# Performance work log

Hardware: AMD Instinct MI355X
Metric: run time of the kernel (lower is better)

Reference implementation:

```python
import jax, jax.numpy as jnp
import numpy as np

N_NODES = 30000
N_EDGES = 480000
T_STEPS = 8
F_IN = 8
HID = 32
K = 5
PERIODS = 8


def setup_inputs() -> dict:
    key = jax.random.key(0)
    ks = jax.random.split(key, 9)
    timesteps = jax.random.normal(ks[0], (T_STEPS, N_NODES, F_IN), jnp.float32)
    src = jax.random.randint(ks[1], (N_EDGES,), 0, N_NODES)
    dst = jax.random.randint(ks[2], (N_EDGES,), 0, N_NODES)
    edge_index = jnp.stack([src, dst])
    # ChebConv weights for gates [i, f, c, o]; glorot-ish scale
    Wx = jax.random.normal(ks[3], (4, K, F_IN, HID), jnp.float32) * (1.0 / np.sqrt(F_IN))
    Wh = jax.random.normal(ks[4], (4, K, HID, HID), jnp.float32) * (1.0 / np.sqrt(HID))
    w_c = jax.random.normal(ks[5], (3, HID), jnp.float32) * 0.1  # peepholes for i, f, o
    b_gates = jax.random.normal(ks[6], (4, HID), jnp.float32) * 0.1  # b_i, b_f, b_c, b_o
    W_lin = jax.random.normal(ks[7], (PERIODS, HID), jnp.float32) * (1.0 / np.sqrt(HID))
    b_lin = jax.random.normal(ks[8], (PERIODS,), jnp.float32) * 0.1
    return {"timesteps": timesteps, "edge_index": edge_index, "Wx": Wx, "Wh": Wh,
            "w_c": w_c, "b_gates": b_gates, "W_lin": W_lin, "b_lin": b_lin}


def reference(timesteps, edge_index, Wx, Wh, w_c, b_gates, W_lin, b_lin):
    N = timesteps.shape[1]
    src, dst = edge_index[0], edge_index[1]
    # get_laplacian('sym') removes self loops, deg over edge rows; with lambda_max=2,
    # L_hat = 2L/lmax - I = -D^{-1/2} A D^{-1/2} (diag: 1 from L plus added -1 self loop = 0)
    w = jnp.where(src != dst, 1.0, 0.0).astype(timesteps.dtype)
    deg = jax.ops.segment_sum(w, src, num_segments=N)
    dis = jnp.where(deg > 0, 1.0 / jnp.sqrt(jnp.where(deg > 0, deg, 1.0)), 0.0)
    norm = dis[src] * w * dis[dst]  # [E]

    def lap(x):  # x: [N, C] -> L_hat @ x
        return -jax.ops.segment_sum(norm[:, None] * x[src], dst, num_segments=N)

    def cheb(x, W):  # Chebyshev recurrence; W: [K, in, out]
        Tx0 = x
        out = Tx0 @ W[0]
        Tx1 = lap(Tx0)
        out = out + Tx1 @ W[1]
        for k in range(2, W.shape[0]):
            Tx2 = 2.0 * lap(Tx1) - Tx0
            out = out + Tx2 @ W[k]
            Tx0, Tx1 = Tx1, Tx2
        return out

    def step(carry, x):
        H, C = carry
        I = jax.nn.sigmoid(cheb(x, Wx[0]) + cheb(H, Wh[0]) + w_c[0] * C + b_gates[0])
        Fg = jax.nn.sigmoid(cheb(x, Wx[1]) + cheb(H, Wh[1]) + w_c[1] * C + b_gates[1])
        Tg = jnp.tanh(cheb(x, Wx[2]) + cheb(H, Wh[2]) + b_gates[2])
        Cn = Fg * C + I * Tg
        O = jax.nn.sigmoid(cheb(x, Wx[3]) + cheb(H, Wh[3]) + w_c[2] * Cn + b_gates[3])
        Hn = O * jnp.tanh(Cn)
        return (Hn, Cn), None

    hid = Wh.shape[-1]
    H0 = jnp.zeros((N, hid), timesteps.dtype)
    (H, C), _ = jax.lax.scan(step, (H0, H0), timesteps)
    return jax.nn.relu(H) @ W_lin.T + b_lin
```

## Files before the change

kernel.cpp:

```cpp
#include <hip/hip_runtime.h>
#include <hip/hip_fp16.h>
#include <math.h>

#define T_STEPS 8
#define F_IN    8
#define HID     32
#define KCH     5
#define PERIODS 8
#define NB      64

typedef __attribute__((ext_vector_type(8))) _Float16 half8_t;
typedef __attribute__((ext_vector_type(4))) float    f32x4_t;

__device__ __forceinline__ float sigmoidf_(float x) { return 1.f / (1.f + __expf(-x)); }
__device__ __forceinline__ float tanhf_(float x) {
    float e = __expf(2.f * x);
    return 1.f - 2.f / (e + 1.f);
}


__global__ void k_count(const int* __restrict__ src, const int* __restrict__ dst,
                        int* __restrict__ degi, int* __restrict__ cnt, int E) {
    int e = blockIdx.x * blockDim.x + threadIdx.x;
    if (e >= E) return;
    int s = src[e], d = dst[e];
    if (s != d) {
        atomicAdd(&degi[s], 1);
        atomicAdd(&cnt[d], 1);
    }
}

__global__ void k_hist2(const int* __restrict__ cnt, int* __restrict__ hist,
                        int N, int NT) {
    __shared__ int h[256];
    int tid = threadIdx.x, blk = blockIdx.x;
    h[tid] = 0;
    __syncthreads();
    int n = blk * 256 + tid;
    if (n < N) atomicAdd(&h[min(cnt[n], 255)], 1);
    __syncthreads();
    hist[tid * NT + blk] = h[tid];
}

__global__ void __launch_bounds__(1024) k_scan(const int* __restrict__ in,
                                               int* __restrict__ outp, int n) {
    __shared__ int wsum[16];
    int tid = threadIdx.x;
    int base = tid * 32;
    int v[32];
    int s = 0;
    #pragma unroll
    for (int i = 0; i < 32; ++i) {
        int idx = base + i;
        int t = (idx < n) ? in[idx] : 0;
        v[i] = t; s += t;
    }
    int lane = tid & 63, wave = tid >> 6;
    int incl = s;
    #pragma unroll
    for (int off = 1; off < 64; off <<= 1) {
        int t = __shfl_up(incl, off, 64);
        if (lane >= off) incl += t;
    }
    if (lane == 63) wsum[wave] = incl;
    __syncthreads();
    if (tid < 64) {
        int w = (tid < 16) ? wsum[tid] : 0;
        int iw = w;
        #pragma unroll
        for (int off = 1; off < 16; off <<= 1) {
            int t = __shfl_up(iw, off, 64);
            if (tid >= off) iw += t;
        }
        if (tid < 16) wsum[tid] = iw - w;
    }
    __syncthreads();
    int excl = wsum[wave] + (incl - s);
    #pragma unroll
    for (int i = 0; i < 32; ++i) {
        int idx = base + i;
        if (idx < n) outp[idx] = excl;
        excl += v[i];
    }
    if (tid == 1023) outp[n] = wsum[15] + incl;
}

__global__ void k_permscat2(const int* __restrict__ cnt, const int* __restrict__ degi,
                            const int* __restrict__ histbase,
                            int* __restrict__ perm, int* __restrict__ iperm,
                            int* __restrict__ cntp, float* __restrict__ dis,
                            int N, int NT) {
    __shared__ int key[256];
    int tid = threadIdx.x, blk = blockIdx.x;
    int n = blk * 256 + tid;
    int k = (n < N) ? min(cnt[n], 255) : -1;
    key[tid] = k;
    __syncthreads();
    if (n < N) {
        int r = 0;
        for (int j = 0; j < tid; ++j) r += (key[j] == k);
        int pos = histbase[k * NT + blk] + r;
        perm[pos] = n;
        iperm[n] = pos;
        cntp[pos] = cnt[n];
        int dg = degi[n];
        dis[n] = (dg > 0) ? rsqrtf((float)dg) : 0.f;
    }
}

__global__ void k_scatxt(const int* __restrict__ src, const int* __restrict__ dst,
                         const float* __restrict__ dis, const int* __restrict__ rowptr,
                         const int* __restrict__ iperm, int* __restrict__ fill,
                         unsigned int* __restrict__ cv, const float* __restrict__ xall,
                         __half* __restrict__ xb,
                         const float* __restrict__ Wh, __half* __restrict__ Bpack,
                         const float* __restrict__ Wx, __half* __restrict__ Bxpack,
                         int N, int E) {
    int gsz = (int)(gridDim.x * blockDim.x);
    int gtid = blockIdx.x * blockDim.x + threadIdx.x;
    for (int e = gtid; e < E; e += gsz) {
        int s = src[e], d = dst[e];
        if (s != d) {
            float nv = -dis[s] * dis[d];
            unsigned short h16 = __half_as_ushort(__float2half(nv));
            int dp = iperm[d];
            int p = atomicAdd(&fill[dp], 1);
            cv[rowptr[dp] + p] = (unsigned int)(unsigned short)iperm[s]
                               | ((unsigned int)h16 << 16);
        }
    }
    for (int i = gtid; i < N * T_STEPS; i += gsz) {
        int n = i >> 3, t = i & 7;
        float4 a = *(const float4*)(xall + ((size_t)t * N + n) * 8);
        float4 b = *(const float4*)(xall + ((size_t)t * N + n) * 8 + 4);
        __half2 h[4];
        h[0] = __float22half2_rn(make_float2(a.x, a.y));
        h[1] = __float22half2_rn(make_float2(a.z, a.w));
        h[2] = __float22half2_rn(make_float2(b.x, b.y));
        h[3] = __float22half2_rn(make_float2(b.z, b.w));
        *(float4*)(xb + (size_t)iperm[n] * 64 + t * 8) = *(float4*)h;
    }
    for (int i = gtid; i < KCH * 8 * 64 * 8; i += gsz) {
        int j = i & 7, lane = (i >> 3) & 63, nt = (i >> 9) & 7, k = i >> 12;
        int col = lane & 15, quad = lane >> 4;
        int kk = quad * 8 + j;
        int o = nt * 16 + col, g = o >> 5, h = o & 31;
        Bpack[i] = __float2half(Wh[(((g * KCH + k) * 32) + kk) * 32 + h]);
    }
    for (int i = gtid; i < 2 * 8 * 64 * 8; i += gsz) {
        int j = i & 7, lane = (i >> 3) & 63, nt = (i >> 9) & 7, c = i >> 12;
        int col = lane & 15, quad = lane >> 4;
        int kk = c * 32 + quad * 8 + j;
        int kcheb = kk >> 3, ch = kk & 7;
        int o = nt * 16 + col, g = o >> 5, h = o & 31;
        float v = (kcheb < KCH) ? Wx[(((g * KCH + kcheb) * 8) + ch) * 32 + h] : 0.f;
        Bxpack[i] = __float2half(v);
    }
}

template <int C, int ES>
__global__ void __launch_bounds__(256) k_lap_h(__half* __restrict__ outp,
                                               const __half* __restrict__ xin,
                                               const __half* __restrict__ xprev,
                                               float alpha, float beta,
                                               const int* __restrict__ rowptr,
                                               const unsigned int* __restrict__ cv,
                                               int N) {
    constexpr int Q = C / 8;
    constexpr int W = Q * ES;
    int idx = blockIdx.x * 256 + threadIdx.x;
    int node = idx / W;
    int r = idx % W;
    int q = r % Q, s = r / Q;
    if (node >= N) return;
    int beg = rowptr[node], end = rowptr[node + 1];
    float a0 = 0.f, a1 = 0.f, a2 = 0.f, a3 = 0.f, a4 = 0.f, a5 = 0.f, a6 = 0.f, a7 = 0.f;
    #pragma unroll 8
    for (int j = beg + s; j < end; j += ES) {
        unsigned int pv = cv[j];
        int pcol = (int)(pv & 0xffffu);
        float nv = __half2float(__ushort_as_half((unsigned short)(pv >> 16)));
        float4 raw = *(const float4*)(xin + (size_t)pcol * C + q * 8);
        const __half2* h = (const __half2*)&raw;
        float2 f0 = __half22float2(h[0]);
        float2 f1 = __half22float2(h[1]);
        float2 f2 = __half22float2(h[2]);
        float2 f3 = __half22float2(h[3]);
        a0 += nv * f0.x; a1 += nv * f0.y; a2 += nv * f1.x; a3 += nv * f1.y;
        a4 += nv * f2.x; a5 += nv * f2.y; a6 += nv * f3.x; a7 += nv * f3.y;
    }
    #pragma unroll
    for (int m = Q; m < W; m <<= 1) {
        a0 += __shfl_xor(a0, m, 64); a1 += __shfl_xor(a1, m, 64);
        a2 += __shfl_xor(a2, m, 64); a3 += __shfl_xor(a3, m, 64);
        a4 += __shfl_xor(a4, m, 64); a5 += __shfl_xor(a5, m, 64);
        a6 += __shfl_xor(a6, m, 64); a7 += __shfl_xor(a7, m, 64);
    }
    if (s != 0) return;
    size_t off = (size_t)node * C + q * 8;
    float r0 = alpha * a0, r1 = alpha * a1, r2 = alpha * a2, r3 = alpha * a3;
    float r4 = alpha * a4, r5 = alpha * a5, r6 = alpha * a6, r7 = alpha * a7;
    if (beta != 0.f) {
        float4 raw = *(const float4*)(xprev + off);
        const __half2* h = (const __half2*)&raw;
        float2 f0 = __half22float2(h[0]);
        float2 f1 = __half22float2(h[1]);
        float2 f2 = __half22float2(h[2]);
        float2 f3 = __half22float2(h[3]);
        r0 += beta * f0.x; r1 += beta * f0.y; r2 += beta * f1.x; r3 += beta * f1.y;
        r4 += beta * f2.x; r5 += beta * f2.y; r6 += beta * f3.x; r7 += beta * f3.y;
    }
    __half2 o[4];
    o[0] = __float22half2_rn(make_float2(r0, r1));
    o[1] = __float22half2_rn(make_float2(r2, r3));
    o[2] = __float22half2_rn(make_float2(r4, r5));
    o[3] = __float22half2_rn(make_float2(r6, r7));
    *(float4*)(outp + off) = *(float4*)o;
}

__global__ void __launch_bounds__(256) k_lapstep(
    const __half* __restrict__ xb, const __half* __restrict__ TXB,
    __half* __restrict__ THall, float* __restrict__ Cst,
    const __half* __restrict__ Bpack, const __half* __restrict__ Bxpack,
    const float* __restrict__ w_c, const float* __restrict__ bg,
    const float* __restrict__ W_lin, const float* __restrict__ b_lin,
    const int* __restrict__ perm, float* __restrict__ out,
    const int* __restrict__ rowptr, const unsigned int* __restrict__ cv,
    int t, int doOut, int N) {
    __shared__ __half T4s[16 * 32];
    __shared__ float Gs[16 * 128];
    __shared__ float Hs[16 * 33];
    int tid = threadIdx.x;
    int base = blockIdx.x * 16;
    int lane = tid & 63, wv = tid >> 6;
    int col = lane & 15, quad = lane >> 4;

    {
        const __half* T3 = THall + (size_t)3 * N * HID;
        const __half* T2 = THall + (size_t)2 * N * HID;
        int nl = tid >> 4;
        int r = tid & 15;
        int q = r & 3, s = r >> 2;
        int node = base + nl; if (node >= N) node = N - 1;
        int beg = rowptr[node], end = rowptr[node + 1];
        float a0 = 0.f, a1 = 0.f, a2 = 0.f, a3 = 0.f, a4 = 0.f, a5 = 0.f, a6 = 0.f, a7 = 0.f;
        #pragma unroll 8
        for (int j = beg + s; j < end; j += 4) {
            unsigned int pv = cv[j];
            int pcol = (int)(pv & 0xffffu);
            float nv = __half2float(__ushort_as_half((unsigned short)(pv >> 16)));
            float4 raw = *(const float4*)(T3 + (size_t)pcol * HID + q * 8);
            const __half2* h = (const __half2*)&raw;
            float2 f0 = __half22float2(h[0]);
            float2 f1 = __half22float2(h[1]);
            float2 f2 = __half22float2(h[2]);
            float2 f3 = __half22float2(h[3]);
            a0 += nv * f0.x; a1 += nv * f0.y; a2 += nv * f1.x; a3 += nv * f1.y;
            a4 += nv * f2.x; a5 += nv * f2.y; a6 += nv * f3.x; a7 += nv * f3.y;
        }
        #pragma unroll
        for (int m = 4; m < 16; m <<= 1) {
            a0 += __shfl_xor(a0, m, 64); a1 += __shfl_xor(a1, m, 64);
            a2 += __shfl_xor(a2, m, 64); a3 += __shfl_xor(a3, m, 64);
            a4 += __shfl_xor(a4, m, 64); a5 += __shfl_xor(a5, m, 64);
            a6 += __shfl_xor(a6, m, 64); a7 += __shfl_xor(a7, m, 64);
        }
        if (s == 0) {
            float4 raw = *(const float4*)(T2 + (size_t)node * HID + q * 8);
            const __half2* h = (const __half2*)&raw;
            float2 f0 = __half22float2(h[0]);
            float2 f1 = __half22float2(h[1]);
            float2 f2 = __half22float2(h[2]);
            float2 f3 = __half22float2(h[3]);
            __half2 o[4];
            o[0] = __float22half2_rn(make_float2(2.f * a0 - f0.x, 2.f * a1 - f0.y));
            o[1] = __float22half2_rn(make_float2(2.f * a2 - f1.x, 2.f * a3 - f1.y));
            o[2] = __float22half2_rn(make_float2(2.f * a4 - f2.x, 2.f * a5 - f2.y));
            o[3] = __float22half2_rn(make_float2(2.f * a6 - f3.x, 2.f * a7 - f3.y));
            *(float4*)(T4s + nl * 32 + q * 8) = *(float4*)o;
        }
    }
    __syncthreads();

    int node_a = base + col; if (node_a >= N) node_a = N - 1;
    f32x4_t acc[2];
    #pragma unroll
    for (int i = 0; i < 2; ++i) {
        float b = bg[(wv + 4 * i) * 16 + col];
        acc[i][0] = b; acc[i][1] = b; acc[i][2] = b; acc[i][3] = b;
    }
    const half8_t* Bx = (const half8_t*)Bxpack;
    const half8_t* Bp = (const half8_t*)Bpack;
    {
        const __half* sp0 = (quad == 0)
            ? (xb + (size_t)node_a * 64 + t * 8)
            : (TXB + ((size_t)(quad - 1) * N + node_a) * 64 + t * 8);
        half8_t ax0 = *(const half8_t*)sp0;
        half8_t ax1 = {};
        if (quad == 0)
            ax1 = *(const half8_t*)(TXB + ((size_t)3 * N + node_a) * 64 + t * 8);
        #pragma unroll
        for (int i = 0; i < 2; ++i) {
            int nt = wv + 4 * i;
            acc[i] = __builtin_amdgcn_mfma_f32_16x16x32_f16(ax0, Bx[nt * 64 + lane], acc[i], 0, 0, 0);
            acc[i] = __builtin_amdgcn_mfma_f32_16x16x32_f16(ax1, Bx[(8 + nt) * 64 + lane], acc[i], 0, 0, 0);
        }
    }
    #pragma unroll
    for (int k = 0; k < 4; ++k) {
        half8_t a = *(const half8_t*)(THall + ((size_t)k * N + node_a) * 32 + quad * 8);
        #pragma unroll
        for (int i = 0; i < 2; ++i) {
            int nt = wv + 4 * i;
            acc[i] = __builtin_amdgcn_mfma_f32_16x16x32_f16(a, Bp[(k * 8 + nt) * 64 + lane], acc[i], 0, 0, 0);
        }
    }
    {
        half8_t a = *(const half8_t*)(T4s + col * 32 + quad * 8);
        #pragma unroll
        for (int i = 0; i < 2; ++i) {
            int nt = wv + 4 * i;
            acc[i] = __builtin_amdgcn_mfma_f32_16x16x32_f16(a, Bp[(4 * 8 + nt) * 64 + lane], acc[i], 0, 0, 0);
        }
    }

    #pragma unroll
    for (int i = 0; i < 2; ++i) {
        int nt = wv + 4 * i;
        #pragma unroll
        for (int reg = 0; reg < 4; ++reg)
            Gs[(quad * 4 + reg) * 128 + nt * 16 + col] = acc[i][reg];
    }
    __syncthreads();

    #pragma unroll
    for (int pp = 0; pp < 2; ++pp) {
        int p = tid + pp * 256;
        int nl = p >> 5, h = p & 31;
        int node = base + nl;
        if (node < N) {
            const float* g = Gs + nl * 128;
            size_t idx = (size_t)node * 32 + h;
            float Co = Cst[idx];
            float I  = sigmoidf_(g[h]      + w_c[h]      * Co);
            float F  = sigmoidf_(g[32 + h] + w_c[32 + h] * Co);
            float Tg = tanhf_(g[64 + h]);
            float Cn = F * Co + I * Tg;
            float O  = sigmoidf_(g[96 + h] + w_c[64 + h] * Cn);
            float Hn = O * tanhf_(Cn);
            Cst[idx] = Cn;
            THall[idx] = __float2half(Hn);
            if (doOut) Hs[nl * 33 + h] = fmaxf(Hn, 0.f);
        } else if (doOut) {
            Hs[nl * 33 + h] = 0.f;
        }
    }

    if (doOut) {
        __syncthreads();
        if (tid < 128) {
            int nl = tid >> 3, pp = tid & 7;
            int node = base + nl;
            if (node < N) {
                float a0 = b_lin[pp];
                const float* hp = Hs + nl * 33;
                #pragma unroll
                for (int h = 0; h < HID; ++h)
                    a0 += hp[h] * W_lin[pp * HID + h];
                out[(size_t)perm[node] * PERIODS + pp] = a0;
            }
        }
    }
}

__global__ void __launch_bounds__(256) k_stepM(
    const __half* __restrict__ xb, const __half* __restrict__ TXB,
    __half* __restrict__ THall, float* __restrict__ Cst,
    const __half* __restrict__ Bxpack,
    const float* __restrict__ w_c, const float* __restrict__ bg,
    int t, int N) {
    int tid = threadIdx.x;
    int wave = tid >> 6, lane = tid & 63;
    int col = lane & 15, quad = lane >> 4;
    int base = blockIdx.x * NB;
    int node_a = base + wave * 16 + col; if (node_a >= N) node_a = N - 1;
    int nc0 = base + wave * 16 + quad * 4;

    f32x4_t acc[8];
    #pragma unroll
    for (int nt = 0; nt < 8; ++nt) {
        float b = bg[nt * 16 + col];
        acc[nt][0] = b; acc[nt][1] = b; acc[nt][2] = b; acc[nt][3] = b;
    }
    const half8_t* Bx = (const half8_t*)Bxpack;
    {
        const __half* sp0 = (quad == 0)
            ? (xb + (size_t)node_a * 64 + t * 8)
            : (TXB + ((size_t)(quad - 1) * N + node_a) * 64 + t * 8);
        half8_t ax0 = *(const half8_t*)sp0;
        half8_t ax1 = {};
        if (quad == 0)
            ax1 = *(const half8_t*)(TXB + ((size_t)3 * N + node_a) * 64 + t * 8);
        #pragma unroll
        for (int nt = 0; nt < 8; ++nt)
            acc[nt] = __builtin_amdgcn_mfma_f32_16x16x32_f16(ax0, Bx[nt * 64 + lane], acc[nt], 0, 0, 0);
        #pragma unroll
        for (int nt = 0; nt < 8; ++nt)
            acc[nt] = __builtin_amdgcn_mfma_f32_16x16x32_f16(ax1, Bx[(8 + nt) * 64 + lane], acc[nt], 0, 0, 0);
    }
    #pragma unroll
    for (int reg = 0; reg < 4; ++reg) {
        int node = nc0 + reg;
        if (node < N) {
            #pragma unroll
            for (int b = 0; b < 2; ++b) {
                int h = col + 16 * b;
                size_t idx = (size_t)node * 32 + h;
                float I  = sigmoidf_(acc[0 + b][reg]);
                float Tg = tanhf_(acc[4 + b][reg]);
                float Cn = I * Tg;
                float O  = sigmoidf_(acc[6 + b][reg] + w_c[64 + h] * Cn);
                Cst[idx] = Cn;
                THall[idx] = __float2half(O * tanhf_(Cn));
            }
        }
    }
}


extern "C" void kernel_launch(void* const* d_in, const int* in_sizes, int n_in,
                              void* d_out, int out_size, void* d_ws, size_t ws_size,
                              hipStream_t stream) {
    const float* xall  = (const float*)d_in[0];
    const int*   ei    = (const int*)d_in[1];
    const float* Wx    = (const float*)d_in[2];
    const float* Wh    = (const float*)d_in[3];
    const float* w_c   = (const float*)d_in[4];
    const float* bg    = (const float*)d_in[5];
    const float* W_lin = (const float*)d_in[6];
    const float* b_lin = (const float*)d_in[7];
    float* out = (float*)d_out;

    const int E = in_sizes[1] / 2;
    const int N = in_sizes[0] / (T_STEPS * F_IN);
    const int NT = (N + 255) / 256;
    const int* src = ei;
    const int* dst = ei + E;

    char* p = (char*)d_ws;
    auto carve = [&](size_t bytes) -> void* {
        void* r = (void*)p;
        p += (bytes + 255) & ~(size_t)255;
        return r;
    };
    char* zero_begin = p;
    int*    degi  = (int*)   carve((size_t)N * 4);
    int*    cnt   = (int*)   carve((size_t)N * 4);
    int*    fill  = (int*)   carve((size_t)N * 4);
    float*  Cst   = (float*) carve((size_t)N * HID * 4);
    size_t zero_bytes = (size_t)(p - zero_begin);
    __half* THall = (__half*)carve((size_t)4 * N * HID * 2);
    int*    hist     = (int*)   carve((size_t)256 * NT * 4);
    int*    histbase = (int*)   carve(((size_t)256 * NT + 1) * 4);
    float*  dis      = (float*) carve((size_t)N * 4);
    int*    perm     = (int*)   carve((size_t)N * 4);
    int*    iperm    = (int*)   carve((size_t)N * 4);
    int*    cntp     = (int*)   carve((size_t)N * 4);
    int*    rowptr   = (int*)   carve((size_t)(N + 1) * 4);
    unsigned int* cv = (unsigned int*)carve((size_t)E * 4);
    __half* xb       = (__half*)carve((size_t)N * 64 * 2);
    __half* TXB      = (__half*)carve((size_t)4 * N * 64 * 2);
    __half* Bpack    = (__half*)carve((size_t)KCH * 8 * 64 * 8 * 2);
    __half* Bxpack   = (__half*)carve((size_t)2 * 8 * 64 * 8 * 2);

    hipMemsetAsync(zero_begin, 0, zero_bytes, stream);

    const int TB = 256;
    const int gE = (E + TB - 1) / TB;
    k_count<<<gE, TB, 0, stream>>>(src, dst, degi, cnt, E);
    k_hist2<<<NT, TB, 0, stream>>>(cnt, hist, N, NT);
    k_scan<<<1, 1024, 0, stream>>>(hist, histbase, 256 * NT);
    k_permscat2<<<NT, TB, 0, stream>>>(cnt, degi, histbase, perm, iperm, cntp, dis, N, NT);
    k_scan<<<1, 1024, 0, stream>>>(cntp, rowptr, N);
    k_scatxt<<<gE, TB, 0, stream>>>(src, dst, dis, rowptr, iperm, fill, cv, xall, xb,
                                    Wh, Bpack, Wx, Bxpack, N, E);

    __half* TXB0 = TXB;
    __half* TXB1 = TXB + (size_t)N * 64;
    __half* TXB2 = TXB + (size_t)2 * N * 64;
    __half* TXB3 = TXB + (size_t)3 * N * 64;
    const int lapx_grid = (N * 32 + TB - 1) / TB;
    k_lap_h<64, 4><<<lapx_grid, TB, 0, stream>>>(TXB0, xb,   nullptr, 1.f,  0.f, rowptr, cv, N);
    k_lap_h<64, 4><<<lapx_grid, TB, 0, stream>>>(TXB1, TXB0, xb,      2.f, -1.f, rowptr, cv, N);
    k_lap_h<64, 4><<<lapx_grid, TB, 0, stream>>>(TXB2, TXB1, TXB0,    2.f, -1.f, rowptr, cv, N);
    k_lap_h<64, 4><<<lapx_grid, TB, 0, stream>>>(TXB3, TXB2, TXB1,    2.f, -1.f, rowptr, cv, N);

    const int laph_grid = (N * 16 + TB - 1) / TB;
    const int lapstep_grid = (N + 15) / 16;
    __half* TH0 = THall;
    __half* TH1 = THall + (size_t)N * HID;
    __half* TH2 = THall + (size_t)2 * N * HID;
    __half* TH3 = THall + (size_t)3 * N * HID;

    k_stepM<<<(N + NB - 1) / NB, TB, 0, stream>>>(xb, TXB, THall, Cst, Bxpack,
                                                  w_c, bg, 0, N);

    for (int t = 1; t < T_STEPS; ++t) {
        k_lap_h<HID, 4><<<laph_grid, TB, 0, stream>>>(TH1, TH0, nullptr, 1.f,  0.f, rowptr, cv, N);
        k_lap_h<HID, 4><<<laph_grid, TB, 0, stream>>>(TH2, TH1, TH0,     2.f, -1.f, rowptr, cv, N);
        k_lap_h<HID, 4><<<laph_grid, TB, 0, stream>>>(TH3, TH2, TH1,     2.f, -1.f, rowptr, cv, N);
        k_lapstep<<<lapstep_grid, TB, 0, stream>>>(xb, TXB, THall, Cst, Bpack, Bxpack,
                                                   w_c, bg, W_lin, b_lin, perm, out,
                                                   rowptr, cv, t,
                                                   (t == T_STEPS - 1) ? 1 : 0, N);
    }
}
```

Measured before the change: 614.3 us.

## Precompute two-hop Laplacian to compute first two Chebyshev hidden terms in parallel

Builds an explicit L² sparse matrix by expanding each row's neighbours' neighbour lists. Each recurrent step then computes T1 = L·H and T2 = 2·L²·H − H in one combined launch, removing one dependent Laplacian pass per step. It also folds the last input Chebyshev term into the t=0 step kernel. In exchange, L² has roughly deg² entries per row, so each step does far more gather work. There is also a per-call setup cost to build the two-hop structure and a large extra buffer.

```diff
diff --git a/kernel.cpp b/kernel.cpp
--- a/kernel.cpp
+++ b/kernel.cpp
@@ -155,6 +155,42 @@
         int o = nt * 16 + col, g = o >> 5, h = o & 31;
         float v = (kcheb < KCH) ? Wx[(((g * KCH + kcheb) * 8) + ch) * 32 + h] : 0.f;
         Bxpack[i] = __float2half(v);
+    }
+}
+
+__global__ void k_off2(const int* __restrict__ rowptr, const unsigned int* __restrict__ cv,
+                       int* __restrict__ eoffrel, int* __restrict__ rowidx,
+                       int* __restrict__ deg2, int N) {
+    int i = blockIdx.x * blockDim.x + threadIdx.x;
+    if (i >= N) return;
+    int beg = rowptr[i], end = rowptr[i + 1];
+    int off = 0;
+    for (int e = beg; e < end; ++e) {
+        int j = (int)(cv[e] & 0xffffu);
+        eoffrel[e] = off;
+        rowidx[e] = i;
+        off += rowptr[j + 1] - rowptr[j];
+    }
+    deg2[i] = off;
+}
+
+__global__ void k_copy2(const int* __restrict__ rowptr, const unsigned int* __restrict__ cv,
+                        const int* __restrict__ eoffrel, const int* __restrict__ rowidx,
+                        const int* __restrict__ rowptr2, unsigned int* __restrict__ cv2,
+                        int N, int E) {
+    int e = blockIdx.x * blockDim.x + threadIdx.x;
+    if (e >= rowptr[N]) return;
+    unsigned int pv = cv[e];
+    int j = (int)(pv & 0xffffu);
+    float wij = __half2float(__ushort_as_half((unsigned short)(pv >> 16)));
+    int i = rowidx[e];
+    unsigned int* dstp = cv2 + rowptr2[i] + eoffrel[e];
+    int jb = rowptr[j], je = rowptr[j + 1];
+    for (int kp = jb; kp < je; ++kp) {
+        unsigned int kv = cv[kp];
+        float wjk = __half2float(__ushort_as_half((unsigned short)(kv >> 16)));
+        unsigned short pw = __half_as_ushort(__float2half(wij * wjk));
+        dstp[kp - jb] = (kv & 0xffffu) | ((unsigned int)pw << 16);
     }
 }
 
@@ -218,6 +254,95 @@
     *(float4*)(outp + off) = *(float4*)o;
 }
 
+__global__ void __launch_bounds__(256) k_lapAB(
+    __half* __restrict__ T1, __half* __restrict__ T2, const __half* __restrict__ H,
+    const int* __restrict__ rowptr, const unsigned int* __restrict__ cv,
+    const int* __restrict__ rowptr2, const unsigned int* __restrict__ cv2,
+    int B1, int N) {
+    int bid = blockIdx.x;
+    int tid = threadIdx.x;
+    if (bid < B1) {
+        int idx = bid * 256 + tid;
+        int node = idx >> 4;
+        int r = idx & 15;
+        int q = r & 3, s = r >> 2;
+        if (node >= N) return;
+        int beg = rowptr[node], end = rowptr[node + 1];
+        float a0 = 0.f, a1 = 0.f, a2 = 0.f, a3 = 0.f, a4 = 0.f, a5 = 0.f, a6 = 0.f, a7 = 0.f;
+        #pragma unroll 8
+        for (int j = beg + s; j < end; j += 4) {
+            unsigned int pv = cv[j];
+            int pcol = (int)(pv & 0xffffu);
+            float nv = __half2float(__ushort_as_half((unsigned short)(pv >> 16)));
+            float4 raw = *(const float4*)(H + (size_t)pcol * HID + q * 8);
+            const __half2* h = (const __half2*)&raw;
+            float2 f0 = __half22float2(h[0]);
+            float2 f1 = __half22float2(h[1]);
+            float2 f2 = __half22float2(h[2]);
+            float2 f3 = __half22float2(h[3]);
+            a0 += nv * f0.x; a1 += nv * f0.y; a2 += nv * f1.x; a3 += nv * f1.y;
+            a4 += nv * f2.x; a5 += nv * f2.y; a6 += nv * f3.x; a7 += nv * f3.y;
+        }
+        #pragma unroll
+        for (int m = 4; m < 16; m <<= 1) {
+            a0 += __shfl_xor(a0, m, 64); a1 += __shfl_xor(a1, m, 64);
+            a2 += __shfl_xor(a2, m, 64); a3 += __shfl_xor(a3, m, 64);
+            a4 += __shfl_xor(a4, m, 64); a5 += __shfl_xor(a5, m, 64);
+            a6 += __shfl_xor(a6, m, 64); a7 += __shfl_xor(a7, m, 64);
+        }
+        if (s != 0) return;
+        __half2 o[4];
+        o[0] = __float22half2_rn(make_float2(a0, a1));
+        o[1] = __float22half2_rn(make_float2(a2, a3));
+        o[2] = __float22half2_rn(make_float2(a4, a5));
+        o[3] = __float22half2_rn(make_float2(a6, a7));
+        *(float4*)(T1 + (size_t)node * HID + q * 8) = *(float4*)o;
+    } else {
+        int idx = (bid - B1) * 256 + tid;
+        int node = idx >> 6;
+        int r = idx & 63;
+        int q = r & 3, s = r >> 2;
+        if (node >= N) return;
+        int beg = rowptr2[node], end = rowptr2[node + 1];
+        float a0 = 0.f, a1 = 0.f, a2 = 0.f, a3 = 0.f, a4 = 0.f, a5 = 0.f, a6 = 0.f, a7 = 0.f;
+        #pragma unroll 8
+        for (int j = beg + s; j < end; j += 16) {
+            unsigned int pv = cv2[j];
+            int pcol = (int)(pv & 0xffffu);
+            float nv = __half2float(__ushort_as_half((unsigned short)(pv >> 16)));
+            float4 raw = *(const float4*)(H + (size_t)pcol * HID + q * 8);
+            const __half2* h = (const __half2*)&raw;
+            float2 f0 = __half22float2(h[0]);
+            float2 f1 = __half22float2(h[1]);
+            float2 f2 = __half22float2(h[2]);
+            float2 f3 = __half22float2(h[3]);
+            a0 += nv * f0.x; a1 += nv * f0.y; a2 += nv * f1.x; a3 += nv * f1.y;
+            a4 += nv * f2.x; a5 += nv * f2.y; a6 += nv * f3.x; a7 += nv * f3.y;
+        }
+        #pragma unroll
+        for (int m = 4; m < 64; m <<= 1) {
+            a0 += __shfl_xor(a0, m, 64); a1 += __shfl_xor(a1, m, 64);
+            a2 += __shfl_xor(a2, m, 64); a3 += __shfl_xor(a3, m, 64);
+            a4 += __shfl_xor(a4, m, 64); a5 += __shfl_xor(a5, m, 64);
+            a6 += __shfl_xor(a6, m, 64); a7 += __shfl_xor(a7, m, 64);
+        }
+        if (s != 0) return;
+        size_t off = (size_t)node * HID + q * 8;
+        float4 raw = *(const float4*)(H + off);
+        const __half2* h = (const __half2*)&raw;
+        float2 f0 = __half22float2(h[0]);
+        float2 f1 = __half22float2(h[1]);
+        float2 f2 = __half22float2(h[2]);
+        float2 f3 = __half22float2(h[3]);
+        __half2 o[4];
+        o[0] = __float22half2_rn(make_float2(2.f * a0 - f0.x, 2.f * a1 - f0.y));
+        o[1] = __float22half2_rn(make_float2(2.f * a2 - f1.x, 2.f * a3 - f1.y));
+        o[2] = __float22half2_rn(make_float2(2.f * a4 - f2.x, 2.f * a5 - f2.y));
+        o[3] = __float22half2_rn(make_float2(2.f * a6 - f3.x, 2.f * a7 - f3.y));
+        *(float4*)(T2 + off) = *(float4*)o;
+    }
+}
+
 __global__ void __launch_bounds__(256) k_lapstep(
     const __half* __restrict__ xb, const __half* __restrict__ TXB,
     __half* __restrict__ THall, float* __restrict__ Cst,
@@ -373,56 +498,112 @@
     }
 }
 
-__global__ void __launch_bounds__(256) k_stepM(
+__global__ void __launch_bounds__(256) k_lapstep0(
     const __half* __restrict__ xb, const __half* __restrict__ TXB,
-    __half* __restrict__ THall, float* __restrict__ Cst,
+    __half* __restrict__ TXB3, __half* __restrict__ THall, float* __restrict__ Cst,
     const __half* __restrict__ Bxpack,
     const float* __restrict__ w_c, const float* __restrict__ bg,
-    int t, int N) {
+    const int* __restrict__ rowptr, const unsigned int* __restrict__ cv, int N) {
+    __shared__ __half X3s[16 * 64];
+    __shared__ float Gs[16 * 128];
     int tid = threadIdx.x;
-    int wave = tid >> 6, lane = tid & 63;
+    int base = blockIdx.x * 16;
+    int lane = tid & 63, wv = tid >> 6;
     int col = lane & 15, quad = lane >> 4;
-    int base = blockIdx.x * NB;
-    int node_a = base + wave * 16 + col; if (node_a >= N) node_a = N - 1;
-    int nc0 = base + wave * 16 + quad * 4;
-
-    f32x4_t acc[8];
-    #pragma unroll
-    for (int nt = 0; nt < 8; ++nt) {
-        float b = bg[nt * 16 + col];
-        acc[nt][0] = b; acc[nt][1] = b; acc[nt][2] = b; acc[nt][3] = b;
+
+    {
+        const __half* T2 = TXB + (size_t)2 * N * 64;
+        const __half* T1 = TXB + (size_t)1 * N * 64;
+        int nl = tid >> 4;
+        int r = tid & 15;
+        int q = r & 7, s = r >> 3;
+        int node = base + nl; if (node >= N) node = N - 1;
+        int beg = rowptr[node], end = rowptr[node + 1];
+        float a0 = 0.f, a1 = 0.f, a2 = 0.f, a3 = 0.f, a4 = 0.f, a5 = 0.f, a6 = 0.f, a7 = 0.f;
+        #pragma unroll 8
+        for (int j = beg + s; j < end; j += 2) {
+            unsigned int pv = cv[j];
+            int pcol = (int)(pv & 0xffffu);
+            float nv = __half2float(__ushort_as_half((unsigned short)(pv >> 16)));
+            float4 raw = *(const float4*)(T2 + (size_t)pcol * 64 + q * 8);
+            const __half2* h = (const __half2*)&raw;
+            float2 f0 = __half22float2(h[0]);
+            float2 f1 = __half22float2(h[1]);
+            float2 f2 = __half22float2(h[2]);
+            float2 f3 = __half22float2(h[3]);
+            a0 += nv * f0.x; a1 += nv * f0.y; a2 += nv * f1.x; a3 += nv * f1.y;
+            a4 += nv * f2.x; a5 += nv * f2.y; a6 += nv * f3.x; a7 += nv * f3.y;
+        }
+        a0 += __shfl_xor(a0, 8, 64); a1 += __shfl_xor(a1, 8, 64);
+        a2 += __shfl_xor(a2, 8, 64); a3 += __shfl_xor(a3, 8, 64);
+        a4 += __shfl_xor(a4, 8, 64); a5 += __shfl_xor(a5, 8, 64);
+        a6 += __shfl_xor(a6, 8, 64); a7 += __shfl_xor(a7, 8, 64);
+        if (s == 0) {
+            size_t off = (size_t)node * 64 + q * 8;
+            float4 raw = *(const float4*)(T1 + off);
+            const __half2* h = (const __half2*)&raw;
+            float2 f0 = __half22float2(h[0]);
+            float2 f1 = __half22float2(h[1]);
+            float2 f2 = __half22float2(h[2]);
+            float2 f3 = __half22float2(h[3]);
+            __half2 o[4];
+            o[0] = __float22half2_rn(make_float2(2.f * a0 - f0.x, 2.f * a1 - f0.y));
+            o[1] = __float22half2_rn(make_float2(2.f * a2 - f1.x, 2.f * a3 - f1.y));
+            o[2] = __float22half2_rn(make_float2(2.f * a4 - f2.x, 2.f * a5 - f2.y));
+            o[3] = __float22half2_rn(make_float2(2.f * a6 - f3.x, 2.f * a7 - f3.y));
+            *(float4*)(TXB3 + off) = *(float4*)o;
+            *(float4*)(X3s + nl * 64 + q * 8) = *(float4*)o;
+        }
+    }
+    __syncthreads();
+
+    int node_a = base + col; if (node_a >= N) node_a = N - 1;
+    f32x4_t acc[2];
+    #pragma unroll
+    for (int i = 0; i < 2; ++i) {
+        float b = bg[(wv + 4 * i) * 16 + col];
+        acc[i][0] = b; acc[i][1] = b; acc[i][2] = b; acc[i][3] = b;
     }
     const half8_t* Bx = (const half8_t*)Bxpack;
     {
         const __half* sp0 = (quad == 0)
-            ? (xb + (size_t)node_a * 64 + t * 8)
-            : (TXB + ((size_t)(quad - 1) * N + node_a) * 64 + t * 8);
+            ? (xb + (size_t)node_a * 64)
+            : (TXB + ((size_t)(quad - 1) * N + node_a) * 64);
         half8_t ax0 = *(const half8_t*)sp0;
         half8_t ax1 = {};
         if (quad == 0)
-            ax1 = *(const half8_t*)(TXB + ((size_t)3 * N + node_a) * 64 + t * 8);
-        #pragma unroll
-        for (int nt = 0; nt < 8; ++nt)
-            acc[nt] = __builtin_amdgcn_mfma_f32_16x16x32_f16(ax0, Bx[nt * 64 + lane], acc[nt], 0, 0, 0);
-        #pragma unroll
-        for (int nt = 0; nt < 8; ++nt)
-            acc[nt] = __builtin_amdgcn_mfma_f32_16x16x32_f16(ax1, Bx[(8 + nt) * 64 + lane], acc[nt], 0, 0, 0);
-    }
-    #pragma unroll
-    for (int reg = 0; reg < 4; ++reg) {
-        int node = nc0 + reg;
+            ax1 = *(const half8_t*)(X3s + col * 64);
+        #pragma unroll
+        for (int i = 0; i < 2; ++i) {
+            int nt = wv + 4 * i;
+            acc[i] = __builtin_amdgcn_mfma_f32_16x16x32_f16(ax0, Bx[nt * 64 + lane], acc[i], 0, 0, 0);
+            acc[i] = __builtin_amdgcn_mfma_f32_16x16x32_f16(ax1, Bx[(8 + nt) * 64 + lane], acc[i], 0, 0, 0);
+        }
+    }
+
+    #pragma unroll
+    for (int i = 0; i < 2; ++i) {
+        int nt = wv + 4 * i;
+        #pragma unroll
+        for (int reg = 0; reg < 4; ++reg)
+            Gs[(quad * 4 + reg) * 128 + nt * 16 + col] = acc[i][reg];
+    }
+    __syncthreads();
+
+    #pragma unroll
+    for (int pp = 0; pp < 2; ++pp) {
+        int p = tid + pp * 256;
+        int nl = p >> 5, h = p & 31;
+        int node = base + nl;
         if (node < N) {
-            #pragma unroll
-            for (int b = 0; b < 2; ++b) {
-                int h = col + 16 * b;
-                size_t idx = (size_t)node * 32 + h;
-                float I  = sigmoidf_(acc[0 + b][reg]);
-                float Tg = tanhf_(acc[4 + b][reg]);
-                float Cn = I * Tg;
-                float O  = sigmoidf_(acc[6 + b][reg] + w_c[64 + h] * Cn);
-                Cst[idx] = Cn;
-                THall[idx] = __float2half(O * tanhf_(Cn));
-            }
+            const float* g = Gs + nl * 128;
+            size_t idx = (size_t)node * 32 + h;
+            float I  = sigmoidf_(g[h]);
+            float Tg = tanhf_(g[64 + h]);
+            float Cn = I * Tg;
+            float O  = sigmoidf_(g[96 + h] + w_c[64 + h] * Cn);
+            Cst[idx] = Cn;
+            THall[idx] = __float2half(O * tanhf_(Cn));
         }
     }
 }
@@ -472,11 +653,17 @@
     __half* TXB      = (__half*)carve((size_t)4 * N * 64 * 2);
     __half* Bpack    = (__half*)carve((size_t)KCH * 8 * 64 * 8 * 2);
     __half* Bxpack   = (__half*)carve((size_t)2 * 8 * 64 * 8 * 2);
+    int*    eoffrel  = (int*)   carve((size_t)E * 4);
+    int*    rowidx   = (int*)   carve((size_t)E * 4);
+    int*    deg2     = (int*)   carve((size_t)N * 4);
+    int*    rowptr2  = (int*)   carve((size_t)(N + 1) * 4);
+    unsigned int* cv2 = (unsigned int*)carve((size_t)16 * 1024 * 1024 * 4);
 
     hipMemsetAsync(zero_begin, 0, zero_bytes, stream);
 
     const int TB = 256;
     const int gE = (E + TB - 1) / TB;
+    const int gN = (N + TB - 1) / TB;
     k_count<<<gE, TB, 0, stream>>>(src, dst, degi, cnt, E);
     k_hist2<<<NT, TB, 0, stream>>>(cnt, hist, N, NT);
     k_scan<<<1, 1024, 0, stream>>>(hist, histbase, 256 * NT);
@@ -484,6 +671,9 @@
     k_scan<<<1, 1024, 0, stream>>>(cntp, rowptr, N);
     k_scatxt<<<gE, TB, 0, stream>>>(src, dst, dis, rowptr, iperm, fill, cv, xall, xb,
                                     Wh, Bpack, Wx, Bxpack, N, E);
+    k_off2<<<gN, TB, 0, stream>>>(rowptr, cv, eoffrel, rowidx, deg2, N);
+    k_scan<<<1, 1024, 0, stream>>>(deg2, rowptr2, N);
+    k_copy2<<<gE, TB, 0, stream>>>(rowptr, cv, eoffrel, rowidx, rowptr2, cv2, N, E);
 
     __half* TXB0 = TXB;
     __half* TXB1 = TXB + (size_t)N * 64;
@@ -493,22 +683,23 @@
     k_lap_h<64, 4><<<lapx_grid, TB, 0, stream>>>(TXB0, xb,   nullptr, 1.f,  0.f, rowptr, cv, N);
     k_lap_h<64, 4><<<lapx_grid, TB, 0, stream>>>(TXB1, TXB0, xb,      2.f, -1.f, rowptr, cv, N);
     k_lap_h<64, 4><<<lapx_grid, TB, 0, stream>>>(TXB2, TXB1, TXB0,    2.f, -1.f, rowptr, cv, N);
-    k_lap_h<64, 4><<<lapx_grid, TB, 0, stream>>>(TXB3, TXB2, TXB1,    2.f, -1.f, rowptr, cv, N);
-
-    const int laph_grid = (N * 16 + TB - 1) / TB;
+
     const int lapstep_grid = (N + 15) / 16;
     __half* TH0 = THall;
     __half* TH1 = THall + (size_t)N * HID;
     __half* TH2 = THall + (size_t)2 * N * HID;
     __half* TH3 = THall + (size_t)3 * N * HID;
 
-    k_stepM<<<(N + NB - 1) / NB, TB, 0, stream>>>(xb, TXB, THall, Cst, Bxpack,
-                                                  w_c, bg, 0, N);
+    k_lapstep0<<<lapstep_grid, TB, 0, stream>>>(xb, TXB, TXB3, THall, Cst, Bxpack,
+                                                w_c, bg, rowptr, cv, N);
+
+    const int B1 = (N * 16 + TB - 1) / TB;
+    const int B2 = (N * 64 + TB - 1) / TB;
+    const int laph_grid = (N * 16 + TB - 1) / TB;
 
     for (int t = 1; t < T_STEPS; ++t) {
-        k_lap_h<HID, 4><<<laph_grid, TB, 0, stream>>>(TH1, TH0, nullptr, 1.f,  0.f, rowptr, cv, N);
-        k_lap_h<HID, 4><<<laph_grid, TB, 0, stream>>>(TH2, TH1, TH0,     2.f, -1.f, rowptr, cv, N);
-        k_lap_h<HID, 4><<<laph_grid, TB, 0, stream>>>(TH3, TH2, TH1,     2.f, -1.f, rowptr, cv, N);
+        k_lapAB<<<B1 + B2, TB, 0, stream>>>(TH1, TH2, TH0, rowptr, cv, rowptr2, cv2, B1, N);
+        k_lap_h<HID, 4><<<laph_grid, TB, 0, stream>>>(TH3, TH2, TH1, 2.f, -1.f, rowptr, cv, N);
         k_lapstep<<<lapstep_grid, TB, 0, stream>>>(xb, TXB, THall, Cst, Bpack, Bxpack,
                                                    w_c, bg, W_lin, b_lin, perm, out,
                                                    rowptr, cv, t,
```

Result: slower. 896.6 us (+45.9%).
